# Performance work log

Measured on AMD Instinct MI355X. Metric: run time of the kernel, lower is better.

## Reference

```python
import jax, jax.numpy as jnp
import numpy as np

SHAPE0 = (256, 256)   # top pyramid level (h, w)
SIGMA = 3.0
EPS = 1e-3
BATCH = 128
N_CHAN = 3
N_LEVELS = 4
N_PIX = sum((SHAPE0[0] >> i) * (SHAPE0[1] >> i) for i in range(N_LEVELS))  # 87040


def _gauss_lum_kernel(sigma):
    # 2D Gaussian times RGB luminance weights -> HWIO kernel (kh, kw, 3, 1)
    s = int(np.ceil(2 * sigma))
    u = np.linspace(-s, s, 2 * s + 1)
    g = np.exp(-(u[:, None] ** 2 + u[None, :] ** 2) / (2 * sigma ** 2)) / (2 * np.pi * sigma ** 2)
    w = np.array([0.2989, 0.587, 0.114])
    k = (g[:, :, None, None] * w[None, None, :, None]).astype(np.float32)
    return jnp.asarray(k)


def _conv_same(x, k):
    # NHWC conv with zero 'SAME' padding; equivalent to the original
    # pad(s) + SAME conv + center crop (net effect is SAME with zero pad).
    return jax.lax.conv_general_dilated(
        x, k, window_strides=(1, 1), padding='SAME',
        dimension_numbers=('NHWC', 'HWIO', 'NHWC'))


def setup_inputs() -> dict:
    key = jax.random.key(0)
    x = jax.random.uniform(key, (BATCH, N_PIX, N_CHAN), dtype=jnp.float32)
    return {"x": x}


def reference(x):
    k = _gauss_lum_kernel(SIGMA)
    n_pix, nc = x.shape[1], x.shape[2]
    h, w = SHAPE0
    outs = []
    i = 0
    while i + h * w <= n_pix:  # static Python loop over pyramid levels
        xi = x[:, i:i + h * w, :].reshape(-1, h, w, nc)          # (B,h,w,3)
        lum = _conv_same(xi, k)                                   # (B,h,w,1)
        dens = _conv_same(jnp.ones((1, h, w, nc), x.dtype), k)    # (1,h,w,1), input-independent
        outs.append((xi / (lum / dens + EPS)).reshape(-1, h * w, nc))
        i += h * w
        h //= 2
        w //= 2
    return jnp.concatenate(outs, axis=1)  # packed pyramid (B, n_pix, 3)
```

## Files before the change

kernel.cpp:

```cpp
#include <hip/hip_runtime.h>


#define NPIX   87040
#define EPSV   1e-3f
#define WSUM   0.9999f
#define TW     64
#define TH     16
#define RAD    6
#define LW     80
#define LH     28
#define NG     (LH * 20)
#define NBLK   11008
#define NXCD   8
#define CHUNK  (NBLK / NXCD)

__device__ __constant__ float G1[13] = {
    0.01799699f, 0.03315904f, 0.05467002f, 0.08065689f, 0.10648267f,
    0.12579441f, 0.13298076f, 0.12579441f, 0.10648267f, 0.08065689f,
    0.05467002f, 0.03315904f, 0.01799699f
};
__device__ __constant__ float PRE[14] = {
    0.00000000f, 0.01799699f, 0.05115603f, 0.10582605f, 0.18648294f,
    0.29296561f, 0.41876002f, 0.55174078f, 0.67753519f, 0.78401786f,
    0.86467475f, 0.91934477f, 0.95250381f, 0.97050080f
};

__global__ __launch_bounds__(256)
void mslln_kernel(const float* __restrict__ x, float* __restrict__ out) {
    __shared__ float s_lum[LH][LW];
    __shared__ float s_rc[LH][TW];
    __shared__ float s_scale[TH][TW];

    const int bphys = blockIdx.x;
    const int bid   = (bphys & (NXCD - 1)) * CHUNK + (bphys >> 3);
    const int t     = threadIdx.x;

    int img, tl, txlog, h, off;
    if (bid < 8192)       { img = bid >> 6;                 tl = bid & 63; txlog = 2; h = 256; off = 0;     }
    else if (bid < 10240) { int r = bid - 8192;  img = r >> 4; tl = r & 15; txlog = 1; h = 128; off = 65536; }
    else if (bid < 10752) { int r = bid - 10240; img = r >> 2; tl = r & 3;  txlog = 0; h = 64;  off = 81920; }
    else                  { int r = bid - 10752; img = r >> 1; tl = r & 1;  txlog = 0; h = 32;  off = 86016; }
    const int w   = h;
    const int tx0 = (tl & ((1 << txlog) - 1)) << 6;
    const int ty0 = (tl >> txlog) << 4;

    const float* __restrict__ xb = x   + (size_t)img * (NPIX * 3) + (size_t)off * 3;
    float*       __restrict__ ob = out + (size_t)img * (NPIX * 3) + (size_t)off * 3;

#pragma unroll
    for (int k = 0; k < 3; k++) {
        unsigned i = t + k * 256;
        if (i < NG) {
            int gr  = i / 20;
            int gc  = i - gr * 20;
            int gy  = ty0 + gr - RAD;
            int gx0 = tx0 + (gc << 2) - 8;
            float4 f0 = {0,0,0,0}, f1 = {0,0,0,0}, f2 = {0,0,0,0};
            if (gy >= 0 && gy < h) {
                if (gx0 >= 0 && gx0 + 3 < w) {
                    const float4* p = (const float4*)(xb + ((size_t)gy * w + gx0) * 3);
                    f0 = p[0]; f1 = p[1]; f2 = p[2];
                } else {
                    float v[12];
#pragma unroll
                    for (int c = 0; c < 12; c++) v[c] = 0.f;
#pragma unroll
                    for (int c = 0; c < 4; c++) {
                        int gx = gx0 + c;
                        if (gx >= 0 && gx < w) {
                            const float* s = xb + ((size_t)gy * w + gx) * 3;
                            v[3*c] = s[0]; v[3*c+1] = s[1]; v[3*c+2] = s[2];
                        }
                    }
                    f0 = make_float4(v[0], v[1], v[2],  v[3]);
                    f1 = make_float4(v[4], v[5], v[6],  v[7]);
                    f2 = make_float4(v[8], v[9], v[10], v[11]);
                }
            }
            float l0 = 0.2989f*f0.x + 0.587f*f0.y + 0.114f*f0.z;
            float l1 = 0.2989f*f0.w + 0.587f*f1.x + 0.114f*f1.y;
            float l2 = 0.2989f*f1.z + 0.587f*f1.w + 0.114f*f2.x;
            float l3 = 0.2989f*f2.y + 0.587f*f2.z + 0.114f*f2.w;
            *(float4*)&s_lum[gr][gc << 2] = make_float4(l0, l1, l2, l3);
        }
    }
    __syncthreads();

#pragma unroll
    for (int k = 0; k < 7; k++) {
        int i = t + k * 256;
        int r = i >> 6, c = i & 63;
        float s = 0.f;
#pragma unroll
        for (int j = 0; j < 13; j++) s += s_lum[r][c + 2 + j] * G1[j];
        s_rc[r][c] = s;
    }
    __syncthreads();

#pragma unroll
    for (int k = 0; k < 4; k++) {
        int i  = t + k * 256;
        int ly = i >> 6, lx = i & 63;
        if (tx0 + lx < w) {
            float s = 0.f;
#pragma unroll
            for (int j = 0; j < 13; j++) s += s_rc[ly + j][lx] * G1[j];
            int gy = ty0 + ly, gx = tx0 + lx;
            int ylo = min(RAD, gy), yhi = min(RAD, h - 1 - gy);
            int xlo = min(RAD, gx), xhi = min(RAD, w - 1 - gx);
            float Sy = PRE[RAD + yhi + 1] - PRE[RAD - ylo];
            float Sx = PRE[RAD + xhi + 1] - PRE[RAD - xlo];
            float dens = WSUM * Sy * Sx;
            s_scale[ly][lx] = 1.0f / (s / dens + EPSV);
        }
    }
    __syncthreads();

    {
        int gr  = t >> 4;
        int gc  = t & 15;
        int gx0 = tx0 + (gc << 2);
        if (gx0 < w) {
            int gy = ty0 + gr;
            const float4* p = (const float4*)(xb + ((size_t)gy * w + gx0) * 3);
            float4 f0 = p[0], f1 = p[1], f2 = p[2];
            float4 sc = *(const float4*)&s_scale[gr][gc << 2];
            f0.x *= sc.x; f0.y *= sc.x; f0.z *= sc.x; f0.w *= sc.y;
            f1.x *= sc.y; f1.y *= sc.y; f1.z *= sc.z; f1.w *= sc.z;
            f2.x *= sc.z; f2.y *= sc.w; f2.z *= sc.w; f2.w *= sc.w;
            float4* q = (float4*)(ob + ((size_t)gy * w + gx0) * 3);
            q[0] = f0; q[1] = f1; q[2] = f2;
        }
    }
}

extern "C" void kernel_launch(void* const* d_in, const int* in_sizes, int n_in,
                              void* d_out, int out_size, void* d_ws, size_t ws_size,
                              hipStream_t stream) {
    const float* x = (const float*)d_in[0];
    float* out = (float*)d_out;
    mslln_kernel<<<NBLK, 256, 0, stream>>>(x, out);
}
```

Before: 245.4 us.

## Register-block separable blur, prefetch output pixels early, alias shared buffers

The horizontal and vertical blur passes now compute four outputs per thread from float4 shared-memory loads held in registers, which cuts LDS traffic. Padded strides are added to reduce bank conflicts. The center pixels needed for the final scaling are loaded from global memory before the blur, so that load latency overlaps the convolution work. The scale buffer reuses the luminance buffer's shared memory, shrinking LDS use and possibly raising occupancy. The division is rewritten as dens/(s+eps*dens), which adds register pressure from the prefetched values.

```diff
diff --git a/kernel.cpp b/kernel.cpp
--- a/kernel.cpp
+++ b/kernel.cpp
@@ -8,6 +8,8 @@
 #define TH     16
 #define RAD    6
 #define LW     80
+#define LWP    84
+#define RCP    68
 #define LH     28
 #define NG     (LH * 20)
 #define NBLK   11008
@@ -27,9 +29,10 @@
 
 __global__ __launch_bounds__(256)
 void mslln_kernel(const float* __restrict__ x, float* __restrict__ out) {
-    __shared__ float s_lum[LH][LW];
-    __shared__ float s_rc[LH][TW];
-    __shared__ float s_scale[TH][TW];
+    __shared__ float s_mem[LH * LWP];
+    __shared__ float s_rc[LH][RCP];
+    float (*s_lum)[LWP]   = (float(*)[LWP])s_mem;
+    float (*s_scale)[RCP] = (float(*)[RCP])s_mem;
 
     const int bphys = blockIdx.x;
     const int bid   = (bphys & (NXCD - 1)) * CHUNK + (bphys >> 3);
@@ -86,51 +89,78 @@
     }
     __syncthreads();
 
-#pragma unroll
-    for (int k = 0; k < 7; k++) {
-        int i = t + k * 256;
-        int r = i >> 6, c = i & 63;
-        float s = 0.f;
-#pragma unroll
-        for (int j = 0; j < 13; j++) s += s_lum[r][c + 2 + j] * G1[j];
-        s_rc[r][c] = s;
+    const int p4_gr  = t >> 4;
+    const int p4_gc  = t & 15;
+    const int p4_gx0 = tx0 + (p4_gc << 2);
+    float4 f0p = {0,0,0,0}, f1p = {0,0,0,0}, f2p = {0,0,0,0};
+    if (p4_gx0 < w) {
+        const float4* p = (const float4*)(xb + ((size_t)(ty0 + p4_gr) * w + p4_gx0) * 3);
+        f0p = p[0]; f1p = p[1]; f2p = p[2];
     }
-    __syncthreads();
 
 #pragma unroll
-    for (int k = 0; k < 4; k++) {
-        int i  = t + k * 256;
-        int ly = i >> 6, lx = i & 63;
-        if (tx0 + lx < w) {
-            float s = 0.f;
+    for (int k = 0; k < 2; k++) {
+        int gi = t + (k << 8);
+        if (gi < 448) {
+            int r  = gi >> 4;
+            int c4 = (gi & 15) << 2;
+            float a[20];
 #pragma unroll
-            for (int j = 0; j < 13; j++) s += s_rc[ly + j][lx] * G1[j];
-            int gy = ty0 + ly, gx = tx0 + lx;
-            int ylo = min(RAD, gy), yhi = min(RAD, h - 1 - gy);
-            int xlo = min(RAD, gx), xhi = min(RAD, w - 1 - gx);
-            float Sy = PRE[RAD + yhi + 1] - PRE[RAD - ylo];
-            float Sx = PRE[RAD + xhi + 1] - PRE[RAD - xlo];
-            float dens = WSUM * Sy * Sx;
-            s_scale[ly][lx] = 1.0f / (s / dens + EPSV);
+            for (int m = 0; m < 5; m++)
+                *(float4*)&a[m << 2] = *(const float4*)&s_lum[r][c4 + (m << 2)];
+            float s0 = 0.f, s1 = 0.f, s2 = 0.f, s3 = 0.f;
+#pragma unroll
+            for (int j = 0; j < 13; j++) {
+                float gj = G1[j];
+                s0 += a[2 + j] * gj;
+                s1 += a[3 + j] * gj;
+                s2 += a[4 + j] * gj;
+                s3 += a[5 + j] * gj;
+            }
+            *(float4*)&s_rc[r][c4] = make_float4(s0, s1, s2, s3);
         }
     }
     __syncthreads();
 
     {
-        int gr  = t >> 4;
-        int gc  = t & 15;
-        int gx0 = tx0 + (gc << 2);
-        if (gx0 < w) {
-            int gy = ty0 + gr;
-            const float4* p = (const float4*)(xb + ((size_t)gy * w + gx0) * 3);
-            float4 f0 = p[0], f1 = p[1], f2 = p[2];
-            float4 sc = *(const float4*)&s_scale[gr][gc << 2];
-            f0.x *= sc.x; f0.y *= sc.x; f0.z *= sc.x; f0.w *= sc.y;
-            f1.x *= sc.y; f1.y *= sc.y; f1.z *= sc.z; f1.w *= sc.z;
-            f2.x *= sc.z; f2.y *= sc.w; f2.z *= sc.w; f2.w *= sc.w;
-            float4* q = (float4*)(ob + ((size_t)gy * w + gx0) * 3);
-            q[0] = f0; q[1] = f1; q[2] = f2;
+        int ly  = t >> 4;
+        int lx4 = (t & 15) << 2;
+        if (tx0 + lx4 < w) {
+            float4 acc = {0.f, 0.f, 0.f, 0.f};
+#pragma unroll
+            for (int j = 0; j < 13; j++) {
+                float4 v = *(const float4*)&s_rc[ly + j][lx4];
+                float gj = G1[j];
+                acc.x += v.x * gj; acc.y += v.y * gj;
+                acc.z += v.z * gj; acc.w += v.w * gj;
+            }
+            int gy = ty0 + ly;
+            int ylo = min(RAD, gy), yhi = min(RAD, h - 1 - gy);
+            float Sy = PRE[RAD + yhi + 1] - PRE[RAD - ylo];
+            float4 sc;
+#pragma unroll
+            for (int d = 0; d < 4; d++) {
+                int gx = tx0 + lx4 + d;
+                int xlo = min(RAD, gx), xhi = min(RAD, w - 1 - gx);
+                float Sx = PRE[RAD + xhi + 1] - PRE[RAD - xlo];
+                float dens = WSUM * Sy * Sx;
+                float s = (d == 0) ? acc.x : (d == 1) ? acc.y : (d == 2) ? acc.z : acc.w;
+                float r = dens / (s + EPSV * dens);
+                if (d == 0) sc.x = r; else if (d == 1) sc.y = r;
+                else if (d == 2) sc.z = r; else sc.w = r;
+            }
+            *(float4*)&s_scale[ly][lx4] = sc;
         }
+    }
+    __syncthreads();
+
+    if (p4_gx0 < w) {
+        float4 sc = *(const float4*)&s_scale[p4_gr][p4_gc << 2];
+        f0p.x *= sc.x; f0p.y *= sc.x; f0p.z *= sc.x; f0p.w *= sc.y;
+        f1p.x *= sc.y; f1p.y *= sc.y; f1p.z *= sc.z; f1p.w *= sc.z;
+        f2p.x *= sc.z; f2p.y *= sc.w; f2p.z *= sc.w; f2p.w *= sc.w;
+        float4* q = (float4*)(ob + ((size_t)(ty0 + p4_gr) * w + p4_gx0) * 3);
+        q[0] = f0p; q[1] = f1p; q[2] = f2p;
     }
 }
 
```

Measured after the change: 243.9 us. No clear change (-0.6%).
